# Kernel optimization log

Measured on AMD Instinct MI355X. Metric: run time of the kernel, lower is better.

Reference implementation:

```python
import jax, jax.numpy as jnp
import numpy as np

N_NODES = 200   # sensors
SEQ = 128       # sequence_length == d_model of per-node transformers
BATCH = 256     # transformer treats batch as the attention sequence (2D input)
HEADS = 4
LAYERS = 2
NF = 1          # num_features (forced to 1 by fc dims)
F_OUT = 64      # num_out_features
G_OUT = 64      # gnn_output_dim
N_EDGES = 1600
D = SEQ
EPS = 1e-5


def setup_inputs() -> dict:
    key = jax.random.key(0)
    ks = jax.random.split(key, 20)
    s = 0.05
    nrm = lambda k, shp: jax.random.normal(k, shp, jnp.float32) * s
    return {
        "x": jax.random.normal(ks[0], (BATCH, N_NODES, SEQ), jnp.float32),
        "edge_index": jax.random.randint(ks[1], (2, N_EDGES), 0, N_NODES),
        # per-node, per-layer transformer params (stacked for vmap)
        "Wqkv": nrm(ks[2], (N_NODES, LAYERS, 3 * D, D)),
        "bqkv": nrm(ks[3], (N_NODES, LAYERS, 3 * D)),
        "Wo": nrm(ks[4], (N_NODES, LAYERS, D, D)),
        "bo": nrm(ks[5], (N_NODES, LAYERS, D)),
        "g1": jnp.ones((N_NODES, LAYERS, D), jnp.float32),
        "be1": jnp.zeros((N_NODES, LAYERS, D), jnp.float32),
        "fW1": nrm(ks[6], (N_NODES, LAYERS, D, D)),  # dim_feedforward = SEQ = D
        "fb1": nrm(ks[7], (N_NODES, LAYERS, D)),
        "fW2": nrm(ks[8], (N_NODES, LAYERS, D, D)),
        "fb2": nrm(ks[9], (N_NODES, LAYERS, D)),
        "g2": jnp.ones((N_NODES, LAYERS, D), jnp.float32),
        "be2": jnp.zeros((N_NODES, LAYERS, D), jnp.float32),
        # shared fc: Linear(SEQ*NF, F_OUT)
        "fc_W": nrm(ks[10], (F_OUT, SEQ * NF)),
        "fc_b": nrm(ks[11], (F_OUT,)),
        # GATConv(F_OUT, G_OUT), heads=1
        "gat_W": nrm(ks[12], (G_OUT, F_OUT)),
        "att_src": nrm(ks[13], (G_OUT,)),
        "att_dst": nrm(ks[14], (G_OUT,)),
        "gat_b": nrm(ks[15], (G_OUT,)),
        # predictor Linear(G_OUT, 2)
        "pred_W": nrm(ks[16], (2, G_OUT)),
        "pred_b": nrm(ks[17], (2,)),
    }


def _ln(v, g, b):
    m = v.mean(-1, keepdims=True)
    var = ((v - m) ** 2).mean(-1, keepdims=True)
    return (v - m) / jnp.sqrt(var + EPS) * g + b


def _encoder_one_node(xn, Wqkv, bqkv, Wo, bo, g1, be1, fW1, fb1, fW2, fb2, g2, be2):
    # xn: [S, D] with S = BATCH (torch treats the 2D input as unbatched seq)
    dh = D // HEADS
    scale = jnp.asarray(1.0 / np.sqrt(dh), xn.dtype)
    for l in range(LAYERS):  # post-norm TransformerEncoderLayer, relu, no dropout (eval)
        qkv = xn @ Wqkv[l].T + bqkv[l]                    # [S, 3D]
        q, k, v = jnp.split(qkv, 3, axis=-1)
        q = q.reshape(-1, HEADS, dh)
        k = k.reshape(-1, HEADS, dh)
        v = v.reshape(-1, HEADS, dh)
        s = jnp.einsum('qhd,khd->hqk', q, k) * scale      # [H, S, S]
        a = jax.nn.softmax(s, axis=-1)
        o = jnp.einsum('hqk,khd->qhd', a, v).reshape(-1, D)
        o = o @ Wo[l].T + bo[l]
        xn = _ln(xn + o, g1[l], be1[l])
        f = jax.nn.relu(xn @ fW1[l].T + fb1[l]) @ fW2[l].T + fb2[l]
        xn = _ln(xn + f, g2[l], be2[l])
    return xn


def _forward(edge_index, x, Wqkv, bqkv, Wo, bo, g1, be1, fW1, fb1, fW2, fb2, g2, be2,
             fc_W, fc_b, gat_W, att_src, att_dst, gat_b, pred_W, pred_b):
    B, N, _ = x.shape
    xt = jnp.transpose(x, (1, 0, 2))                      # [N, B, D]
    t_out = jax.vmap(_encoder_one_node)(xt, Wqkv, bqkv, Wo, bo, g1, be1,
                                        fW1, fb1, fW2, fb2, g2, be2)  # [N, B, D]
    feat = t_out @ fc_W.T + fc_b                          # [N, B, F_OUT]
    # replicate torch.cat(dim=0) over nodes followed by .view(B, N, F)
    feat = feat.reshape(N * B, F_OUT).reshape(B, N, F_OUT)

    # GATConv with add_self_loops, heads=1, negative_slope=0.2
    loops = jnp.arange(N, dtype=edge_index.dtype)
    src = jnp.concatenate([edge_index[0], loops])
    dst = jnp.concatenate([edge_index[1], loops])

    def gat(h_in):  # h_in: [N, F_OUT]
        h = h_in @ gat_W.T                                # [N, G_OUT]
        a_s = h @ att_src                                 # [N]
        a_d = h @ att_dst
        e = jax.nn.leaky_relu(a_s[src] + a_d[dst], 0.2)   # [E+N]
        emax = jax.ops.segment_max(e, dst, num_segments=N)
        emax = jnp.where(jnp.isfinite(emax), emax, 0.0)
        w = jnp.exp(e - emax[dst])
        denom = jax.ops.segment_sum(w, dst, num_segments=N)
        alpha = w / (denom[dst] + 1e-16)
        return jax.ops.segment_sum(alpha[:, None] * h[src], dst, num_segments=N) + gat_b

    g = jax.vmap(gat)(feat)                               # [B, N, G_OUT]
    return g @ pred_W.T + pred_b                          # [B, N, 2]


def reference(x, edge_index, Wqkv, bqkv, Wo, bo, g1, be1, fW1, fb1, fW2, fb2, g2, be2,
              fc_W, fc_b, gat_W, att_src, att_dst, gat_b, pred_W, pred_b):
    return _forward(edge_index, x, Wqkv, bqkv, Wo, bo, g1, be1, fW1, fb1, fW2, fb2,
                    g2, be2, fc_W, fc_b, gat_W, att_src, att_dst, gat_b, pred_W, pred_b)
```

## Files before the change

### kernel.cpp

```cpp
#include <hip/hip_runtime.h>
#include <hip/hip_bf16.h>

#define NN 200
#define BB 256
#define DD 128
#define DH 32
#define NE 1600
#define LL 2

typedef short short8 __attribute__((ext_vector_type(8)));
typedef short short4a __attribute__((ext_vector_type(4)));
typedef float floatx4 __attribute__((ext_vector_type(4)));
using bf16 = __hip_bfloat16;


__device__ __forceinline__ short bfs(float x) {
  bf16 h = __float2bfloat16(x);
  return *(short*)&h;
}
__device__ __forceinline__ float b2f(short s) {
  union { unsigned u; float f; } cv;
  cv.u = ((unsigned)(unsigned short)s) << 16;
  return cv.f;
}

__device__ __forceinline__ void swz_node(int bid, int per_node, int& node, int& rem) {
  int xcd = bid & 7;
  int slot = bid >> 3;
  int q = slot / per_node;
  node = xcd * (NN >> 3) + q;
  rem = slot - q * per_node;
}

__global__ __launch_bounds__(256) void k_transpose(const float* __restrict__ x,
                                                   bf16* __restrict__ X) {
  int tid = blockIdx.x * 256 + threadIdx.x;
  if (tid >= NN * BB * DD) return;
  int d = tid & (DD - 1);
  int rest = tid >> 7;
  int b = rest & (BB - 1);
  int node = rest >> 8;
  X[tid] = (bf16)x[((size_t)b * NN + node) * DD + d];
}

template <int MTPW>
__global__ __launch_bounds__(256) void k_gemm64(const bf16* __restrict__ A,
                                                const float* __restrict__ W,
                                                const float* __restrict__ bias,
                                                bf16* __restrict__ out, int nout,
                                                int astride, size_t woff, int wns,
                                                size_t boff, int bns, int relu,
                                                int nc_count) {
  __shared__ short WS[64 * 136];
  const int RSPLIT = 4 / MTPW;
  int per_node = nc_count * RSPLIT;
  int node, rem;
  swz_node(blockIdx.x, per_node, node, rem);
  int nc = rem / RSPLIT;
  int rh = rem - nc * RSPLIT;
  int tid = threadIdx.x;

  const float4* w4 = (const float4*)(W + woff + (size_t)node * (size_t)wns +
                                     (size_t)nc * 64 * DD);
  for (int i = tid; i < 2048; i += 256) {
    float4 v = w4[i];
    int row = i >> 5, k = (i & 31) << 2;
    short4a p = {bfs(v.x), bfs(v.y), bfs(v.z), bfs(v.w)};
    *(short4a*)&WS[row * 136 + k] = p;
  }
  __syncthreads();

  int w = tid >> 6, lane = tid & 63, r = lane & 15, quad = lane >> 4;
  int base_row = rh * 128 + w * (MTPW * 16);

  const bf16* arow[MTPW];
#pragma unroll
  for (int mt = 0; mt < MTPW; mt++)
    arow[mt] = A + ((size_t)node * BB + base_row + mt * 16 + r) * (size_t)astride + quad * 8;

  floatx4 acc[MTPW][4];
  floatx4 z = {0.f, 0.f, 0.f, 0.f};
#pragma unroll
  for (int mt = 0; mt < MTPW; mt++)
#pragma unroll
    for (int s = 0; s < 4; s++) acc[mt][s] = z;

#pragma unroll
  for (int k0 = 0; k0 < DD; k0 += 32) {
    short8 bq[4];
#pragma unroll
    for (int s = 0; s < 4; s++)
      bq[s] = *(const short8*)&WS[(s * 16 + r) * 136 + quad * 8 + k0];
#pragma unroll
    for (int mt = 0; mt < MTPW; mt++) {
      short8 af = *(const short8*)(arow[mt] + k0);
#pragma unroll
      for (int s = 0; s < 4; s++)
        acc[mt][s] = __builtin_amdgcn_mfma_f32_16x16x32_bf16(af, bq[s], acc[mt][s], 0, 0, 0);
    }
  }

  const float* bp = bias + boff + (size_t)node * (size_t)bns + nc * 64;
  float bv[4];
#pragma unroll
  for (int s = 0; s < 4; s++) bv[s] = bp[s * 16 + r];

  __syncthreads();
  short* mybw = &WS[w * 1088];
  const size_t obase = (size_t)node * BB + base_row;
#pragma unroll
  for (int mt = 0; mt < MTPW; mt++) {
#pragma unroll
    for (int s = 0; s < 4; s++) {
#pragma unroll
      for (int i = 0; i < 4; i++) {
        float v = acc[mt][s][i] + bv[s];
        if (relu) v = v > 0.f ? v : 0.f;
        mybw[(quad * 4 + i) * 68 + s * 16 + r] = bfs(v);
      }
    }
#pragma unroll
    for (int j = 0; j < 2; j++) {
      int chunk = j * 64 + lane;
      int rowr = chunk >> 3, c8 = chunk & 7;
      short8 o = *(const short8*)&mybw[rowr * 68 + c8 * 8];
      *(short8*)((short*)out + (obase + mt * 16 + rowr) * (size_t)nout + nc * 64 + c8 * 8) = o;
    }
  }
}

__global__ __launch_bounds__(256) void k_lngemm(const bf16* __restrict__ A, int astride,
                                                const float* __restrict__ W,
                                                const float* __restrict__ bias,
                                                bf16* __restrict__ X,
                                                const float* __restrict__ g,
                                                const float* __restrict__ be,
                                                size_t woff, int wns, size_t boff,
                                                int bns, int gstride) {
  __shared__ short WS[128 * 136];
  __shared__ float BB4[4][16][68];
  int node, bt;
  swz_node(blockIdx.x, 4, node, bt);
  int tid = threadIdx.x;

  const float4* w4 = (const float4*)(W + woff + (size_t)node * (size_t)wns);
  for (int i = tid; i < 4096; i += 256) {
    float4 v = w4[i];
    int row = i >> 5, k = (i & 31) << 2;
    short4a p = {bfs(v.x), bfs(v.y), bfs(v.z), bfs(v.w)};
    *(short4a*)&WS[row * 136 + k] = p;
  }
  __syncthreads();

  int w = tid >> 6, lane = tid & 63, r = lane & 15, quad = lane >> 4;
  int row0 = bt * 64 + w * 16;
  const bf16* arow = A + ((size_t)node * BB + row0 + r) * (size_t)astride + quad * 8;

  floatx4 acc[8];
  floatx4 z = {0.f, 0.f, 0.f, 0.f};
#pragma unroll
  for (int s = 0; s < 8; s++) acc[s] = z;

#pragma unroll
  for (int k0 = 0; k0 < DD; k0 += 32) {
    short8 af = *(const short8*)(arow + k0);
#pragma unroll
    for (int s = 0; s < 8; s++) {
      short8 bq = *(const short8*)&WS[(s * 16 + r) * 136 + quad * 8 + k0];
      acc[s] = __builtin_amdgcn_mfma_f32_16x16x32_bf16(af, bq, acc[s], 0, 0, 0);
    }
  }

  const float* bp = bias + boff + (size_t)node * (size_t)bns;
  float bv[8];
#pragma unroll
  for (int s = 0; s < 8; s++) bv[s] = bp[s * 16 + r];

  int rrow = lane >> 2, cg = lane & 3;
  float vv[32];
#pragma unroll
  for (int s = 0; s < 4; s++)
#pragma unroll
    for (int i = 0; i < 4; i++)
      BB4[w][quad * 4 + i][s * 16 + r] = acc[s][i] + bv[s];
  if (cg < 2) {
#pragma unroll
    for (int j = 0; j < 8; j++) {
      float4 t4 = *(const float4*)&BB4[w][rrow][(cg & 1) * 32 + j * 4];
      vv[j * 4 + 0] = t4.x; vv[j * 4 + 1] = t4.y;
      vv[j * 4 + 2] = t4.z; vv[j * 4 + 3] = t4.w;
    }
  }
#pragma unroll
  for (int s = 0; s < 4; s++)
#pragma unroll
    for (int i = 0; i < 4; i++)
      BB4[w][quad * 4 + i][s * 16 + r] = acc[s + 4][i] + bv[s + 4];
  if (cg >= 2) {
#pragma unroll
    for (int j = 0; j < 8; j++) {
      float4 t4 = *(const float4*)&BB4[w][rrow][(cg & 1) * 32 + j * 4];
      vv[j * 4 + 0] = t4.x; vv[j * 4 + 1] = t4.y;
      vv[j * 4 + 2] = t4.z; vv[j * 4 + 3] = t4.w;
    }
  }

  size_t xrow = ((size_t)node * BB + row0 + rrow) * DD + cg * 32;
  const short* xr = (const short*)X + xrow;
  float sum = 0.f;
#pragma unroll
  for (int c = 0; c < 4; c++) {
    short8 xs = *(const short8*)(xr + c * 8);
#pragma unroll
    for (int j = 0; j < 8; j++) {
      vv[c * 8 + j] += b2f(xs[j]);
      sum += vv[c * 8 + j];
    }
  }
  sum += __shfl_xor(sum, 1);
  sum += __shfl_xor(sum, 2);
  float mean = sum * (1.0f / 128.0f);
  float vs = 0.f;
#pragma unroll
  for (int j = 0; j < 32; j++) {
    float c = vv[j] - mean;
    vs += c * c;
  }
  vs += __shfl_xor(vs, 1);
  vs += __shfl_xor(vs, 2);
  float inv = rsqrtf(vs * (1.0f / 128.0f) + 1e-5f);

  const float* gp = g + boff + (size_t)node * gstride + cg * 32;
  const float* bep = be + boff + (size_t)node * gstride + cg * 32;
#pragma unroll
  for (int c = 0; c < 4; c++) {
    short8 os;
#pragma unroll
    for (int q2 = 0; q2 < 2; q2++) {
      float4 g4 = *(const float4*)(gp + c * 8 + q2 * 4);
      float4 b4 = *(const float4*)(bep + c * 8 + q2 * 4);
      os[q2 * 4 + 0] = bfs((vv[c * 8 + q2 * 4 + 0] - mean) * inv * g4.x + b4.x);
      os[q2 * 4 + 1] = bfs((vv[c * 8 + q2 * 4 + 1] - mean) * inv * g4.y + b4.y);
      os[q2 * 4 + 2] = bfs((vv[c * 8 + q2 * 4 + 2] - mean) * inv * g4.z + b4.z);
      os[q2 * 4 + 3] = bfs((vv[c * 8 + q2 * 4 + 3] - mean) * inv * g4.w + b4.w);
    }
    *(short8*)((short*)X + xrow + c * 8) = os;
  }
}

__global__ __launch_bounds__(256) void k_attn(bf16* __restrict__ QKV) {
  __shared__ short VT[32 * 264];
  __shared__ short Pw[4 * 2560];
  int node, h;
  swz_node(blockIdx.x, 4, node, h);
  int tid = threadIdx.x;
  int wave = tid >> 6, lane = tid & 63, quad = lane >> 4, l15 = lane & 15;
  short* sbase = (short*)(QKV + (size_t)node * BB * 384);

  for (int i = tid; i < 4096; i += 256) {
    int key = i >> 4, dp = (i & 15) << 1;
    int two = *(const int*)(sbase + (size_t)key * 384 + 256 + h * 32 + dp);
    VT[dp * 264 + key] = (short)(two & 0xffff);
    VT[(dp + 1) * 264 + key] = (short)(((unsigned)two) >> 16);
  }

  int q0 = wave * 64;
  short8 qf[4];
#pragma unroll
  for (int qt = 0; qt < 4; qt++)
    qf[qt] = *(const short8*)(sbase + (size_t)(q0 + qt * 16 + l15) * 384 + h * 32 + quad * 8);

  __syncthreads();

  floatx4 zz = {0.f, 0.f, 0.f, 0.f};
  floatx4 acc[2][4];
#pragma unroll
  for (int dt = 0; dt < 2; dt++)
#pragma unroll
    for (int qt = 0; qt < 4; qt++) acc[dt][qt] = zz;
  float lp[4] = {0.f, 0.f, 0.f, 0.f};
  const float scale = 0.17677669529663689f;
  short* mypw = &Pw[wave * 2560];

  for (int g = 0; g < 8; g++) {
#pragma unroll
    for (int sub = 0; sub < 2; sub++) {
      int kt = g * 2 + sub;
      short8 kf = *(const short8*)(sbase + (size_t)(kt * 16 + l15) * 384 + 128 + h * 32 + quad * 8);
#pragma unroll
      for (int qt = 0; qt < 4; qt++) {
        floatx4 st = __builtin_amdgcn_mfma_f32_16x16x32_bf16(kf, qf[qt], zz, 0, 0, 0);
        float e0 = __expf(st[0] * scale);
        float e1 = __expf(st[1] * scale);
        float e2 = __expf(st[2] * scale);
        float e3 = __expf(st[3] * scale);
        lp[qt] += (e0 + e1) + (e2 + e3);
        short4a p = {bfs(e0), bfs(e1), bfs(e2), bfs(e3)};
        *(short4a*)(mypw + qt * 640 + l15 * 40 + sub * 16 + quad * 4) = p;
      }
    }
    short8 vf0 = *(const short8*)(&VT[l15 * 264 + g * 32 + quad * 8]);
    short8 vf1 = *(const short8*)(&VT[(16 + l15) * 264 + g * 32 + quad * 8]);
#pragma unroll
    for (int qt = 0; qt < 4; qt++) {
      short8 pf = *(const short8*)(mypw + qt * 640 + l15 * 40 + quad * 8);
      acc[0][qt] = __builtin_amdgcn_mfma_f32_16x16x32_bf16(vf0, pf, acc[0][qt], 0, 0, 0);
      acc[1][qt] = __builtin_amdgcn_mfma_f32_16x16x32_bf16(vf1, pf, acc[1][qt], 0, 0, 0);
    }
  }

  float inv[4];
#pragma unroll
  for (int qt = 0; qt < 4; qt++) {
    float lq = lp[qt];
    lq += __shfl_xor(lq, 16);
    lq += __shfl_xor(lq, 32);
    inv[qt] = 1.0f / lq;
  }

#pragma unroll
  for (int qt = 0; qt < 4; qt++)
#pragma unroll
    for (int dt = 0; dt < 2; dt++)
#pragma unroll
      for (int i = 0; i < 4; i++)
        mypw[(qt * 16 + l15) * 40 + dt * 16 + quad * 4 + i] = bfs(acc[dt][qt][i] * inv[qt]);

#pragma unroll
  for (int r = 0; r < 4; r++) {
    int chunk = r * 64 + lane;
    int query = chunk >> 2, d8 = (chunk & 3) * 8;
    short8 o = *(const short8*)(mypw + query * 40 + d8);
    *(short8*)(sbase + (size_t)(q0 + query) * 384 + h * 32 + d8) = o;
  }
}

__global__ __launch_bounds__(256) void k_prep(const float* __restrict__ gatW,
                                              const float* __restrict__ attS,
                                              const float* __restrict__ attD,
                                              const float* __restrict__ predW,
                                              const float* __restrict__ fcW,
                                              const float* __restrict__ fcb,
                                              float* __restrict__ W4,
                                              float* __restrict__ C4) {
  __shared__ float U[4][64];
  int t = threadIdx.x;
  int tt = t >> 6, f = t & 63;
  float u = 0.f;
  if (tt == 0) {
    for (int g = 0; g < 64; g++) u += gatW[g * 64 + f] * attS[g];
  } else if (tt == 1) {
    for (int g = 0; g < 64; g++) u += gatW[g * 64 + f] * attD[g];
  } else if (tt == 2) {
    for (int g = 0; g < 64; g++) u += gatW[g * 64 + f] * predW[g];
  } else {
    for (int g = 0; g < 64; g++) u += gatW[g * 64 + f] * predW[64 + g];
  }
  U[tt][f] = u;
  __syncthreads();
  for (int idx = t; idx < 512; idx += 256) {
    int v = idx >> 7, d = idx & 127;
    float w = 0.f;
#pragma unroll
    for (int ff = 0; ff < 64; ff++) w += fcW[ff * 128 + d] * U[v][ff];
    W4[v * 128 + d] = w;
  }
  if (t < 4) {
    float c = 0.f;
#pragma unroll
    for (int ff = 0; ff < 64; ff++) c += fcb[ff] * U[t][ff];
    C4[t] = c;
  }
}

__global__ __launch_bounds__(256) void k_rows(const bf16* __restrict__ X,
                                              const float* __restrict__ W4,
                                              const float* __restrict__ C4,
                                              float* __restrict__ AS,
                                              float* __restrict__ ADv,
                                              float* __restrict__ HW0,
                                              float* __restrict__ HW1) {
  __shared__ float Wl[512];
  int t = threadIdx.x;
  Wl[t] = W4[t];
  Wl[t + 256] = W4[t + 256];
  __syncthreads();
  int wave = t >> 6, lane = t & 63;
  int rrow = lane >> 3, sub = lane & 7;
  int row = blockIdx.x * 32 + wave * 8 + rrow;
  const short* xp = (const short*)(X + (size_t)row * DD) + sub * 16;
  short8 a = *(const short8*)xp;
  short8 b = *(const short8*)(xp + 8);
  float a0 = 0.f, a1 = 0.f, a2 = 0.f, a3 = 0.f;
#pragma unroll
  for (int j = 0; j < 8; j++) {
    float xf = b2f(a[j]);
    int col = sub * 16 + j;
    a0 += xf * Wl[col];
    a1 += xf * Wl[128 + col];
    a2 += xf * Wl[256 + col];
    a3 += xf * Wl[384 + col];
  }
#pragma unroll
  for (int j = 0; j < 8; j++) {
    float xf = b2f(b[j]);
    int col = sub * 16 + 8 + j;
    a0 += xf * Wl[col];
    a1 += xf * Wl[128 + col];
    a2 += xf * Wl[256 + col];
    a3 += xf * Wl[384 + col];
  }
#pragma unroll
  for (int off = 1; off < 8; off <<= 1) {
    a0 += __shfl_xor(a0, off);
    a1 += __shfl_xor(a1, off);
    a2 += __shfl_xor(a2, off);
    a3 += __shfl_xor(a3, off);
  }
  if (sub == 0) {
    AS[row] = a0 + C4[0];
    ADv[row] = a1 + C4[1];
    HW0[row] = a2 + C4[2];
    HW1[row] = a3 + C4[3];
  }
}

__global__ __launch_bounds__(256) void k_gat(const int* __restrict__ EI,
                                             const float* __restrict__ AS,
                                             const float* __restrict__ ADv,
                                             const float* __restrict__ HW0,
                                             const float* __restrict__ HW1,
                                             const float* __restrict__ gatB,
                                             const float* __restrict__ predW,
                                             const float* __restrict__ predB,
                                             float* __restrict__ OUT) {
  __shared__ float sAS[NN], sAD[NN], sH0[NN], sH1[NN];
  __shared__ float n0[NN], n1[NN], den[NN];
  __shared__ float cc[2];
  int b = blockIdx.x;
  int t = threadIdx.x;
  int base = b * NN;
  for (int i = t; i < NN; i += 256) {
    sAS[i] = AS[base + i];
    sAD[i] = ADv[base + i];
    sH0[i] = HW0[base + i];
    sH1[i] = HW1[base + i];
    n0[i] = 0.f;
    n1[i] = 0.f;
    den[i] = 0.f;
  }
  if (t < 64) {
    float p0 = gatB[t] * predW[t];
    float p1 = gatB[t] * predW[64 + t];
#pragma unroll
    for (int off = 32; off; off >>= 1) {
      p0 += __shfl_down(p0, off);
      p1 += __shfl_down(p1, off);
    }
    if (t == 0) {
      cc[0] = p0 + predB[0];
      cc[1] = p1 + predB[1];
    }
  }
  __syncthreads();

  for (int i = t; i < NE + NN; i += 256) {
    int s, d;
    if (i < NE) {
      s = EI[i];
      d = EI[NE + i];
    } else {
      s = d = i - NE;
    }
    float ev = sAS[s] + sAD[d];
    float lr = ev > 0.f ? ev : 0.2f * ev;
    float w = __expf(lr);
    atomicAdd(&n0[d], w * sH0[s]);
    atomicAdd(&n1[d], w * sH1[s]);
    atomicAdd(&den[d], w);
  }
  __syncthreads();

  for (int i = t; i < NN; i += 256) {
    float inv = 1.0f / (den[i] + 1e-16f);
    OUT[2 * (base + i)] = n0[i] * inv + cc[0];
    OUT[2 * (base + i) + 1] = n1[i] * inv + cc[1];
  }
}

extern "C" void kernel_launch(void* const* d_in, const int* in_sizes, int n_in,
                              void* d_out, int out_size, void* d_ws, size_t ws_size,
                              hipStream_t stream) {
  const float* x = (const float*)d_in[0];
  const int* ei = (const int*)d_in[1];
  const float* Wqkv = (const float*)d_in[2];
  const float* bqkv = (const float*)d_in[3];
  const float* Wo = (const float*)d_in[4];
  const float* bo = (const float*)d_in[5];
  const float* g1 = (const float*)d_in[6];
  const float* be1 = (const float*)d_in[7];
  const float* fW1 = (const float*)d_in[8];
  const float* fb1 = (const float*)d_in[9];
  const float* fW2 = (const float*)d_in[10];
  const float* fb2 = (const float*)d_in[11];
  const float* g2 = (const float*)d_in[12];
  const float* be2 = (const float*)d_in[13];
  const float* fcW = (const float*)d_in[14];
  const float* fcb = (const float*)d_in[15];
  const float* gatW = (const float*)d_in[16];
  const float* attS = (const float*)d_in[17];
  const float* attD = (const float*)d_in[18];
  const float* gatB = (const float*)d_in[19];
  const float* predW = (const float*)d_in[20];
  const float* predB = (const float*)d_in[21];

  const size_t NEED = 52428800;
  if (ws_size < NEED) return;

  char* ws = (char*)d_ws;
  bf16* X = (bf16*)(ws);
  bf16* QKV = (bf16*)(ws + 13107200);
  float* W4 = (float*)(ws + 40960000);
  float* C4 = (float*)(ws + 40962048);
  float* AS = (float*)(ws + 47513600);
  float* ADv = (float*)(ws + 47718400);
  float* HW0 = (float*)(ws + 47923200);
  float* HW1 = (float*)(ws + 48128000);

  k_transpose<<<25600, 256, 0, stream>>>(x, X);

  for (int l = 0; l < LL; l++) {
    size_t w3o = (size_t)l * 384 * DD, b3o = (size_t)l * 384;
    size_t wso = (size_t)l * DD * DD, bso = (size_t)l * DD;
    k_gemm64<4><<<6 * NN, 256, 0, stream>>>(X, Wqkv, bqkv, QKV, 384, DD,
                                            w3o, LL * 384 * DD, b3o, LL * 384, 0, 6);
    k_attn<<<NN * 4, 256, 0, stream>>>(QKV);
    k_lngemm<<<4 * NN, 256, 0, stream>>>(QKV, 384, Wo, bo, X, g1, be1,
                                         wso, LL * DD * DD, bso, LL * DD, LL * DD);
    k_gemm64<2><<<4 * NN, 256, 0, stream>>>(X, fW1, fb1, QKV, 128, DD,
                                            wso, LL * DD * DD, bso, LL * DD, 1, 2);
    k_lngemm<<<4 * NN, 256, 0, stream>>>(QKV, 128, fW2, fb2, X, g2, be2,
                                         wso, LL * DD * DD, bso, LL * DD, LL * DD);
  }

  k_prep<<<1, 256, 0, stream>>>(gatW, attS, attD, predW, fcW, fcb, W4, C4);
  k_rows<<<1600, 256, 0, stream>>>(X, W4, C4, AS, ADv, HW0, HW1);
  k_gat<<<BB, 256, 0, stream>>>(ei, AS, ADv, HW0, HW1, gatB, predW, predB,
                                (float*)d_out);
}
```

Baseline: 496.1 us.

## Fuse final row projection into last LN-GEMM and prefetch operands before weight staging

```diff
diff --git a/kernel.cpp b/kernel.cpp
--- a/kernel.cpp
+++ b/kernel.cpp
@@ -59,6 +59,17 @@
   int nc = rem / RSPLIT;
   int rh = rem - nc * RSPLIT;
   int tid = threadIdx.x;
+  int w = tid >> 6, lane = tid & 63, r = lane & 15, quad = lane >> 4;
+  int base_row = rh * 128 + w * (MTPW * 16);
+
+  short8 areg[MTPW][4];
+#pragma unroll
+  for (int mt = 0; mt < MTPW; mt++) {
+    const bf16* arow =
+        A + ((size_t)node * BB + base_row + mt * 16 + r) * (size_t)astride + quad * 8;
+#pragma unroll
+    for (int k = 0; k < 4; k++) areg[mt][k] = *(const short8*)(arow + k * 32);
+  }
 
   const float4* w4 = (const float4*)(W + woff + (size_t)node * (size_t)wns +
                                      (size_t)nc * 64 * DD);
@@ -70,14 +81,6 @@
   }
   __syncthreads();
 
-  int w = tid >> 6, lane = tid & 63, r = lane & 15, quad = lane >> 4;
-  int base_row = rh * 128 + w * (MTPW * 16);
-
-  const bf16* arow[MTPW];
-#pragma unroll
-  for (int mt = 0; mt < MTPW; mt++)
-    arow[mt] = A + ((size_t)node * BB + base_row + mt * 16 + r) * (size_t)astride + quad * 8;
-
   floatx4 acc[MTPW][4];
   floatx4 z = {0.f, 0.f, 0.f, 0.f};
 #pragma unroll
@@ -86,18 +89,17 @@
     for (int s = 0; s < 4; s++) acc[mt][s] = z;
 
 #pragma unroll
-  for (int k0 = 0; k0 < DD; k0 += 32) {
+  for (int k0 = 0; k0 < 4; k0++) {
     short8 bq[4];
 #pragma unroll
     for (int s = 0; s < 4; s++)
-      bq[s] = *(const short8*)&WS[(s * 16 + r) * 136 + quad * 8 + k0];
-#pragma unroll
-    for (int mt = 0; mt < MTPW; mt++) {
-      short8 af = *(const short8*)(arow[mt] + k0);
+      bq[s] = *(const short8*)&WS[(s * 16 + r) * 136 + quad * 8 + k0 * 32];
+#pragma unroll
+    for (int mt = 0; mt < MTPW; mt++)
 #pragma unroll
       for (int s = 0; s < 4; s++)
-        acc[mt][s] = __builtin_amdgcn_mfma_f32_16x16x32_bf16(af, bq[s], acc[mt][s], 0, 0, 0);
-    }
+        acc[mt][s] = __builtin_amdgcn_mfma_f32_16x16x32_bf16(areg[mt][k0], bq[s],
+                                                             acc[mt][s], 0, 0, 0);
   }
 
   const float* bp = bias + boff + (size_t)node * (size_t)bns + nc * 64;
@@ -136,12 +138,32 @@
                                                 const float* __restrict__ g,
                                                 const float* __restrict__ be,
                                                 size_t woff, int wns, size_t boff,
-                                                int bns, int gstride) {
+                                                int bns, int gstride,
+                                                const float* __restrict__ W4,
+                                                const float* __restrict__ C4,
+                                                float* __restrict__ AS,
+                                                float* __restrict__ ADv,
+                                                float* __restrict__ HW0,
+                                                float* __restrict__ HW1,
+                                                int dofinal) {
   __shared__ short WS[128 * 136];
   __shared__ float BB4[4][16][68];
   int node, bt;
   swz_node(blockIdx.x, 4, node, bt);
   int tid = threadIdx.x;
+  int w = tid >> 6, lane = tid & 63, r = lane & 15, quad = lane >> 4;
+  int row0 = bt * 64 + w * 16;
+  int rrow = lane >> 2, cg = lane & 3;
+
+  const bf16* arow = A + ((size_t)node * BB + row0 + r) * (size_t)astride + quad * 8;
+  short8 areg[4];
+#pragma unroll
+  for (int k = 0; k < 4; k++) areg[k] = *(const short8*)(arow + k * 32);
+  size_t xrow = ((size_t)node * BB + row0 + rrow) * DD + cg * 32;
+  const short* xr = (const short*)X + xrow;
+  short8 xres[4];
+#pragma unroll
+  for (int c = 0; c < 4; c++) xres[c] = *(const short8*)(xr + c * 8);
 
   const float4* w4 = (const float4*)(W + woff + (size_t)node * (size_t)wns);
   for (int i = tid; i < 4096; i += 256) {
@@ -152,22 +174,17 @@
   }
   __syncthreads();
 
-  int w = tid >> 6, lane = tid & 63, r = lane & 15, quad = lane >> 4;
-  int row0 = bt * 64 + w * 16;
-  const bf16* arow = A + ((size_t)node * BB + row0 + r) * (size_t)astride + quad * 8;
-
   floatx4 acc[8];
   floatx4 z = {0.f, 0.f, 0.f, 0.f};
 #pragma unroll
   for (int s = 0; s < 8; s++) acc[s] = z;
 
 #pragma unroll
-  for (int k0 = 0; k0 < DD; k0 += 32) {
-    short8 af = *(const short8*)(arow + k0);
+  for (int k0 = 0; k0 < 4; k0++) {
 #pragma unroll
     for (int s = 0; s < 8; s++) {
-      short8 bq = *(const short8*)&WS[(s * 16 + r) * 136 + quad * 8 + k0];
-      acc[s] = __builtin_amdgcn_mfma_f32_16x16x32_bf16(af, bq, acc[s], 0, 0, 0);
+      short8 bq = *(const short8*)&WS[(s * 16 + r) * 136 + quad * 8 + k0 * 32];
+      acc[s] = __builtin_amdgcn_mfma_f32_16x16x32_bf16(areg[k0], bq, acc[s], 0, 0, 0);
     }
   }
 
@@ -176,7 +193,6 @@
 #pragma unroll
   for (int s = 0; s < 8; s++) bv[s] = bp[s * 16 + r];
 
-  int rrow = lane >> 2, cg = lane & 3;
   float vv[32];
 #pragma unroll
   for (int s = 0; s < 4; s++)
@@ -205,18 +221,14 @@
     }
   }
 
-  size_t xrow = ((size_t)node * BB + row0 + rrow) * DD + cg * 32;
-  const short* xr = (const short*)X + xrow;
   float sum = 0.f;
 #pragma unroll
-  for (int c = 0; c < 4; c++) {
-    short8 xs = *(const short8*)(xr + c * 8);
+  for (int c = 0; c < 4; c++)
 #pragma unroll
     for (int j = 0; j < 8; j++) {
-      vv[c * 8 + j] += b2f(xs[j]);
+      vv[c * 8 + j] += b2f(xres[c][j]);
       sum += vv[c * 8 + j];
     }
-  }
   sum += __shfl_xor(sum, 1);
   sum += __shfl_xor(sum, 2);
   float mean = sum * (1.0f / 128.0f);
@@ -233,18 +245,46 @@
   const float* gp = g + boff + (size_t)node * gstride + cg * 32;
   const float* bep = be + boff + (size_t)node * gstride + cg * 32;
 #pragma unroll
+  for (int c = 0; c < 8; c++) {
+    float4 g4 = *(const float4*)(gp + c * 4);
+    float4 b4 = *(const float4*)(bep + c * 4);
+    vv[c * 4 + 0] = (vv[c * 4 + 0] - mean) * inv * g4.x + b4.x;
+    vv[c * 4 + 1] = (vv[c * 4 + 1] - mean) * inv * g4.y + b4.y;
+    vv[c * 4 + 2] = (vv[c * 4 + 2] - mean) * inv * g4.z + b4.z;
+    vv[c * 4 + 3] = (vv[c * 4 + 3] - mean) * inv * g4.w + b4.w;
+  }
+#pragma unroll
   for (int c = 0; c < 4; c++) {
     short8 os;
 #pragma unroll
-    for (int q2 = 0; q2 < 2; q2++) {
-      float4 g4 = *(const float4*)(gp + c * 8 + q2 * 4);
-      float4 b4 = *(const float4*)(bep + c * 8 + q2 * 4);
-      os[q2 * 4 + 0] = bfs((vv[c * 8 + q2 * 4 + 0] - mean) * inv * g4.x + b4.x);
-      os[q2 * 4 + 1] = bfs((vv[c * 8 + q2 * 4 + 1] - mean) * inv * g4.y + b4.y);
-      os[q2 * 4 + 2] = bfs((vv[c * 8 + q2 * 4 + 2] - mean) * inv * g4.z + b4.z);
-      os[q2 * 4 + 3] = bfs((vv[c * 8 + q2 * 4 + 3] - mean) * inv * g4.w + b4.w);
-    }
+    for (int j = 0; j < 8; j++) os[j] = bfs(vv[c * 8 + j]);
     *(short8*)((short*)X + xrow + c * 8) = os;
+  }
+
+  if (dofinal) {
+    float a0 = 0.f, a1 = 0.f, a2 = 0.f, a3 = 0.f;
+#pragma unroll
+    for (int c = 0; c < 8; c++) {
+      float4 w0 = *(const float4*)(W4 + cg * 32 + c * 4);
+      float4 w1 = *(const float4*)(W4 + 128 + cg * 32 + c * 4);
+      float4 w2 = *(const float4*)(W4 + 256 + cg * 32 + c * 4);
+      float4 w3 = *(const float4*)(W4 + 384 + cg * 32 + c * 4);
+      a0 += vv[c * 4] * w0.x + vv[c * 4 + 1] * w0.y + vv[c * 4 + 2] * w0.z + vv[c * 4 + 3] * w0.w;
+      a1 += vv[c * 4] * w1.x + vv[c * 4 + 1] * w1.y + vv[c * 4 + 2] * w1.z + vv[c * 4 + 3] * w1.w;
+      a2 += vv[c * 4] * w2.x + vv[c * 4 + 1] * w2.y + vv[c * 4 + 2] * w2.z + vv[c * 4 + 3] * w2.w;
+      a3 += vv[c * 4] * w3.x + vv[c * 4 + 1] * w3.y + vv[c * 4 + 2] * w3.z + vv[c * 4 + 3] * w3.w;
+    }
+    a0 += __shfl_xor(a0, 1); a0 += __shfl_xor(a0, 2);
+    a1 += __shfl_xor(a1, 1); a1 += __shfl_xor(a1, 2);
+    a2 += __shfl_xor(a2, 1); a2 += __shfl_xor(a2, 2);
+    a3 += __shfl_xor(a3, 1); a3 += __shfl_xor(a3, 2);
+    if (cg == 0) {
+      int grow = node * BB + row0 + rrow;
+      AS[grow] = a0 + C4[0];
+      ADv[grow] = a1 + C4[1];
+      HW0[grow] = a2 + C4[2];
+      HW1[grow] = a3 + C4[3];
+    }
   }
 }
 
@@ -257,19 +297,18 @@
   int wave = tid >> 6, lane = tid & 63, quad = lane >> 4, l15 = lane & 15;
   short* sbase = (short*)(QKV + (size_t)node * BB * 384);
 
+  int q0 = wave * 64;
+  short8 qf[4];
+#pragma unroll
+  for (int qt = 0; qt < 4; qt++)
+    qf[qt] = *(const short8*)(sbase + (size_t)(q0 + qt * 16 + l15) * 384 + h * 32 + quad * 8);
+
   for (int i = tid; i < 4096; i += 256) {
     int key = i >> 4, dp = (i & 15) << 1;
     int two = *(const int*)(sbase + (size_t)key * 384 + 256 + h * 32 + dp);
     VT[dp * 264 + key] = (short)(two & 0xffff);
     VT[(dp + 1) * 264 + key] = (short)(((unsigned)two) >> 16);
   }
-
-  int q0 = wave * 64;
-  short8 qf[4];
-#pragma unroll
-  for (int qt = 0; qt < 4; qt++)
-    qf[qt] = *(const short8*)(sbase + (size_t)(q0 + qt * 16 + l15) * 384 + h * 32 + quad * 8);
-
   __syncthreads();
 
   floatx4 zz = {0.f, 0.f, 0.f, 0.f};
@@ -282,11 +321,21 @@
   const float scale = 0.17677669529663689f;
   short* mypw = &Pw[wave * 2560];
 
+#define KADDR(kt) (const short8*)(sbase + (size_t)((kt) * 16 + l15) * 384 + 128 + h * 32 + quad * 8)
+  short8 kfA = *KADDR(0);
+  short8 kfB = *KADDR(1);
+
   for (int g = 0; g < 8; g++) {
+    short8 vf0 = *(const short8*)(&VT[l15 * 264 + g * 32 + quad * 8]);
+    short8 vf1 = *(const short8*)(&VT[(16 + l15) * 264 + g * 32 + quad * 8]);
+    short8 nA = kfA, nB = kfB;
+    if (g < 7) {
+      nA = *KADDR(g * 2 + 2);
+      nB = *KADDR(g * 2 + 3);
+    }
 #pragma unroll
     for (int sub = 0; sub < 2; sub++) {
-      int kt = g * 2 + sub;
-      short8 kf = *(const short8*)(sbase + (size_t)(kt * 16 + l15) * 384 + 128 + h * 32 + quad * 8);
+      short8 kf = sub ? kfB : kfA;
 #pragma unroll
       for (int qt = 0; qt < 4; qt++) {
         floatx4 st = __builtin_amdgcn_mfma_f32_16x16x32_bf16(kf, qf[qt], zz, 0, 0, 0);
@@ -299,15 +348,16 @@
         *(short4a*)(mypw + qt * 640 + l15 * 40 + sub * 16 + quad * 4) = p;
       }
     }
-    short8 vf0 = *(const short8*)(&VT[l15 * 264 + g * 32 + quad * 8]);
-    short8 vf1 = *(const short8*)(&VT[(16 + l15) * 264 + g * 32 + quad * 8]);
 #pragma unroll
     for (int qt = 0; qt < 4; qt++) {
       short8 pf = *(const short8*)(mypw + qt * 640 + l15 * 40 + quad * 8);
       acc[0][qt] = __builtin_amdgcn_mfma_f32_16x16x32_bf16(vf0, pf, acc[0][qt], 0, 0, 0);
       acc[1][qt] = __builtin_amdgcn_mfma_f32_16x16x32_bf16(vf1, pf, acc[1][qt], 0, 0, 0);
     }
-  }
+    kfA = nA;
+    kfB = nB;
+  }
+#undef KADDR
 
   float inv[4];
 #pragma unroll
@@ -370,58 +420,6 @@
 #pragma unroll
     for (int ff = 0; ff < 64; ff++) c += fcb[ff] * U[t][ff];
     C4[t] = c;
-  }
-}
-
-__global__ __launch_bounds__(256) void k_rows(const bf16* __restrict__ X,
-                                              const float* __restrict__ W4,
-                                              const float* __restrict__ C4,
-                                              float* __restrict__ AS,
-                                              float* __restrict__ ADv,
-                                              float* __restrict__ HW0,
-                                              float* __restrict__ HW1) {
-  __shared__ float Wl[512];
-  int t = threadIdx.x;
-  Wl[t] = W4[t];
-  Wl[t + 256] = W4[t + 256];
-  __syncthreads();
-  int wave = t >> 6, lane = t & 63;
-  int rrow = lane >> 3, sub = lane & 7;
-  int row = blockIdx.x * 32 + wave * 8 + rrow;
-  const short* xp = (const short*)(X + (size_t)row * DD) + sub * 16;
-  short8 a = *(const short8*)xp;
-  short8 b = *(const short8*)(xp + 8);
-  float a0 = 0.f, a1 = 0.f, a2 = 0.f, a3 = 0.f;
-#pragma unroll
-  for (int j = 0; j < 8; j++) {
-    float xf = b2f(a[j]);
-    int col = sub * 16 + j;
-    a0 += xf * Wl[col];
-    a1 += xf * Wl[128 + col];
-    a2 += xf * Wl[256 + col];
-    a3 += xf * Wl[384 + col];
-  }
-#pragma unroll
-  for (int j = 0; j < 8; j++) {
-    float xf = b2f(b[j]);
-    int col = sub * 16 + 8 + j;
-    a0 += xf * Wl[col];
-    a1 += xf * Wl[128 + col];
-    a2 += xf * Wl[256 + col];
-    a3 += xf * Wl[384 + col];
-  }
-#pragma unroll
-  for (int off = 1; off < 8; off <<= 1) {
-    a0 += __shfl_xor(a0, off);
-    a1 += __shfl_xor(a1, off);
-    a2 += __shfl_xor(a2, off);
-    a3 += __shfl_xor(a3, off);
-  }
-  if (sub == 0) {
-    AS[row] = a0 + C4[0];
-    ADv[row] = a1 + C4[1];
-    HW0[row] = a2 + C4[2];
-    HW1[row] = a3 + C4[3];
   }
 }
 
@@ -514,19 +512,20 @@
   const float* predW = (const float*)d_in[20];
   const float* predB = (const float*)d_in[21];
 
-  const size_t NEED = 52428800;
+  const size_t NEED = 53477376;
   if (ws_size < NEED) return;
 
   char* ws = (char*)d_ws;
   bf16* X = (bf16*)(ws);
   bf16* QKV = (bf16*)(ws + 13107200);
-  float* W4 = (float*)(ws + 40960000);
-  float* C4 = (float*)(ws + 40962048);
-  float* AS = (float*)(ws + 47513600);
-  float* ADv = (float*)(ws + 47718400);
-  float* HW0 = (float*)(ws + 47923200);
-  float* HW1 = (float*)(ws + 48128000);
-
+  float* W4 = (float*)(ws + 52428800);
+  float* C4 = (float*)(ws + 52430848);
+  float* AS = (float*)(ws + 52431872);
+  float* ADv = (float*)(ws + 52636672);
+  float* HW0 = (float*)(ws + 52841472);
+  float* HW1 = (float*)(ws + 53046272);
+
+  k_prep<<<1, 256, 0, stream>>>(gatW, attS, attD, predW, fcW, fcb, W4, C4);
   k_transpose<<<25600, 256, 0, stream>>>(x, X);
 
   for (int l = 0; l < LL; l++) {
@@ -536,15 +535,16 @@
                                             w3o, LL * 384 * DD, b3o, LL * 384, 0, 6);
     k_attn<<<NN * 4, 256, 0, stream>>>(QKV);
     k_lngemm<<<4 * NN, 256, 0, stream>>>(QKV, 384, Wo, bo, X, g1, be1,
-                                         wso, LL * DD * DD, bso, LL * DD, LL * DD);
+                                         wso, LL * DD * DD, bso, LL * DD, LL * DD,
+                                         nullptr, nullptr, nullptr, nullptr,
+                                         nullptr, nullptr, 0);
     k_gemm64<2><<<4 * NN, 256, 0, stream>>>(X, fW1, fb1, QKV, 128, DD,
                                             wso, LL * DD * DD, bso, LL * DD, 1, 2);
     k_lngemm<<<4 * NN, 256, 0, stream>>>(QKV, 128, fW2, fb2, X, g2, be2,
-                                         wso, LL * DD * DD, bso, LL * DD, LL * DD);
-  }
-
-  k_prep<<<1, 256, 0, stream>>>(gatW, attS, attD, predW, fcW, fcb, W4, C4);
-  k_rows<<<1600, 256, 0, stream>>>(X, W4, C4, AS, ADv, HW0, HW1);
+                                         wso, LL * DD * DD, bso, LL * DD, LL * DD,
+                                         W4, C4, AS, ADv, HW0, HW1, (l == LL - 1) ? 1 : 0);
+  }
+
   k_gat<<<BB, 256, 0, stream>>>(ei, AS, ADv, HW0, HW1, gatB, predW, predB,
                                 (float*)d_out);
 }
```

After: 513.2 us. +3.4%, slower.
